# Performance work log

Measured on AMD Instinct MI355X. Metric: run time of the kernel, lower is better.

Reference implementation:

```python
import jax, jax.numpy as jnp
import numpy as np

B, N, E, C1, C2 = 8, 4096, 2048, 128, 128
DENSITY = 0.05  # incidence matrix sparsity (stored dense, as in the original)


def setup_inputs() -> dict:
    key = jax.random.key(0)
    kx, kh, kw = jax.random.split(key, 3)
    x = jax.random.normal(kx, (B, N, C1), dtype=jnp.float32)
    # binary hypergraph incidence matrix [B, n_node, n_edge]
    H = (jax.random.uniform(kh, (B, N, E)) < DENSITY).astype(jnp.float32)
    W = jax.random.normal(kw, (C1, C2), dtype=jnp.float32) * 0.02
    b = jnp.zeros((C2,), dtype=jnp.float32)
    return {"x": x, "H": H, "W": W, "b": b}


def _mean_agg(path, X):
    # path: [B, T, S], X: [B, S, D] -> mean-aggregated [B, T, D]
    out = jnp.matmul(path, X)
    s = jnp.sum(path, axis=2, keepdims=True)  # [B, T, 1]
    # 1/s with inf (s==0) masked to 0, fused as a single where
    return jnp.where(s > 0, out / s, jnp.zeros_like(out))


def reference(x, H, W, b):
    # fc: [B, N, C1] -> [B, N, C2]
    x = jnp.matmul(x, W) + b
    # v2e: aggregate node features into hyperedge features
    Ht = jnp.swapaxes(H, 1, 2)  # [B, E, N]
    e = _mean_agg(Ht, x)        # [B, E, C2]
    # e2v: aggregate hyperedge features back to nodes
    v = _mean_agg(H, e)         # [B, N, C2]
    return v
```

## Files before the change

kernel.cpp:

```cpp
#include <hip/hip_runtime.h>
#include <stdint.h>

constexpr int B_ = 8, N_ = 4096, E_ = 2048, C_ = 128;
constexpr int KT = 32;
constexpr int MT = 64;
constexpr int NJW = 2;

typedef short bf16x8 __attribute__((ext_vector_type(8)));
typedef float f32x4  __attribute__((ext_vector_type(4)));
typedef unsigned int u32x4 __attribute__((ext_vector_type(4)));

__device__ inline uint16_t bf16_rne(float f) {
    uint32_t u = __builtin_bit_cast(uint32_t, f);
    return (uint16_t)((u + 0x7FFFu + ((u >> 16) & 1u)) >> 16);
}

constexpr size_t BIT_B = (size_t)(N_ / 32) * E_;
constexpr size_t HT_E  = (size_t)B_ * BIT_B;
constexpr size_t WT_E  = (size_t)C_ * C_;
constexpr size_t EBF_E = (size_t)B_ * C_ * E_;
constexpr size_t RS_E  = (size_t)B_ * E_;
constexpr size_t RD_E  = (size_t)B_ * N_;

__global__ void pack_kernel(const float* __restrict__ H, uint32_t* __restrict__ HT,
                            uint32_t* __restrict__ HTe) {
    const int t  = threadIdx.x;
    const int eg = blockIdx.x & 7;
    const int ng = (blockIdx.x >> 3) & 127;
    const int b  = blockIdx.x >> 10;
    const int e  = eg * 256 + t;
    const float* hp = H + ((size_t)b * N_ + ng * 32) * E_ + e;
    uint32_t w = 0;
#pragma unroll
    for (int i = 0; i < 32; ++i) w |= (hp[(size_t)i * E_] > 0.5f) ? (1u << i) : 0u;
    HT[((size_t)b * (N_ / 32) + ng) * E_ + e] = w;

    const int lane  = t & 63;
    const int ebase = eg * 256 + (t >> 6) * 64;
    uint32_t val = 0;
#pragma unroll
    for (int i = 0; i < 32; ++i) {
        unsigned long long m = __ballot((w >> i) & 1u);
        uint32_t half = (lane < 32) ? (uint32_t)m : (uint32_t)(m >> 32);
        if ((lane & 31) == i) val = half;
    }
    HTe[((size_t)b * (E_ / 32) + (ebase >> 5) + (lane >> 5)) * N_ + ng * 32 + (lane & 31)] = val;
}

__global__ void prep_kernel(const float* __restrict__ W, const uint32_t* __restrict__ HT,
                            const uint32_t* __restrict__ HTe, uint16_t* __restrict__ WTb,
                            float* __restrict__ rs_e, float* __restrict__ rd_n) {
    const int blk = blockIdx.x, t = threadIdx.x;
    if (blk < 128) {
        const int i = blk * 256 + t;
        const int b = i >> 12, n = i & 4095;
        const uint32_t* p = HTe + (size_t)b * BIT_B + n;
        int s = 0;
#pragma unroll 1
        for (int ew = 0; ew < E_ / 32; ++ew) s += __popc(p[(size_t)ew * N_]);
        rd_n[i] = (s > 0) ? 0.5f / (float)s : 0.f;
    } else if (blk < 192) {
        const int i = (blk - 128) * 256 + t;
        const int b = i >> 11, e = i & 2047;
        const uint32_t* p = HT + (size_t)b * BIT_B + e;
        int s = 0;
#pragma unroll 1
        for (int ng = 0; ng < N_ / 32; ++ng) s += __popc(p[(size_t)ng * E_]);
        rs_e[i] = (s > 0) ? 0.5f / (float)s : 0.f;
    } else if (blk < 256) {
        const int i = (blk - 192) * 256 + t;
        const int c = i >> 7, k = i & 127;
        WTb[i] = bf16_rne(W[k * C_ + c]);
    }
}


#define LOADA(S, k0_) do {                                                            \
    if constexpr (MODE == 0) {                                                        \
        _Pragma("unroll")                                                             \
        for (int g = 0; g < NG; ++g) {                                                \
            const float* ap = Ax + ((size_t)batch * N_ + m0 + g * 16 + l15) * C_ + (k0_) + quad * 8; \
            const float4 f0 = *(const float4*)ap;                                     \
            const float4 f1 = *(const float4*)(ap + 4);                               \
            af##S[g*8+0]=f0.x; af##S[g*8+1]=f0.y; af##S[g*8+2]=f0.z; af##S[g*8+3]=f0.w; \
            af##S[g*8+4]=f1.x; af##S[g*8+5]=f1.y; af##S[g*8+6]=f1.z; af##S[g*8+7]=f1.w; \
        }                                                                             \
    } else {                                                                          \
        const uint32_t* p = Hp + (size_t)((k0_) >> 5) * RL + m0 + l15;                \
        _Pragma("unroll")                                                             \
        for (int g = 0; g < NG; ++g) aw##S[g] = p[g * 16];                            \
    } } while (0)

#define LOADB(S, k0_) do {                                                            \
    _Pragma("unroll")                                                                 \
    for (int j2 = 0; j2 < NJW; ++j2)                                                  \
        bq##S[j2] = *(const bf16x8*)&Bp[(size_t)((jw + j2) * 16 + l15) * K + (k0_) + quad * 8]; \
    } while (0)

#define MKFRAGS(S, A)                                                                 \
    bf16x8 A[NG];                                                                     \
    do {                                                                              \
    if constexpr (MODE == 0) {                                                        \
        _Pragma("unroll")                                                             \
        for (int g = 0; g < NG; ++g)                                                  \
            { _Pragma("unroll")                                                       \
              for (int jj = 0; jj < 8; ++jj) A[g][jj] = (short)bf16_rne(af##S[g*8+jj]); } \
    } else {                                                                          \
        const int qs = quad * 8;                                                      \
        _Pragma("unroll")                                                             \
        for (int g = 0; g < NG; ++g) {                                                \
            const uint32_t wv = aw##S[g];                                             \
            const uint32_t nb0 = (wv >> qs) & 0xFu;                                   \
            const uint32_t nb1 = (wv >> (qs + 4)) & 0xFu;                             \
            const uint32_t s0m = ((nb0 * 0x204081u) & 0x01010101u) << 6;              \
            const uint32_t s1m = ((nb1 * 0x204081u) & 0x01010101u) << 6;              \
            u32x4 qq = { __builtin_amdgcn_perm(s0m, 0u, 0x05000400u),                 \
                         __builtin_amdgcn_perm(s0m, 0u, 0x07000600u),                 \
                         __builtin_amdgcn_perm(s1m, 0u, 0x05000400u),                 \
                         __builtin_amdgcn_perm(s1m, 0u, 0x07000600u) };               \
            A[g] = __builtin_bit_cast(bf16x8, qq);                                    \
        }                                                                             \
    } } while (0)

template <int MODE>
__device__ __attribute__((always_inline))
void gemm_body(const float* __restrict__ Ax, const uint32_t* __restrict__ bits,
               const uint16_t* __restrict__ Btb, const float* __restrict__ bias,
               const float* __restrict__ rcp, uint16_t* __restrict__ outT,
               float* __restrict__ outF) {
    constexpr int K   = (MODE == 0) ? C_ : (MODE == 1) ? N_ : E_;
    constexpr int SW  = K / KT;
    constexpr int OLD = (MODE == 0) ? N_ : E_;
    constexpr int RL  = (MODE == 1) ? E_ : N_;
    constexpr int NG  = MT / 16;
    static_assert(SW >= 4 && SW % 4 == 0, "pipeline needs SW multiple of 4");

    const int t = threadIdx.x, wave = t >> 6, lane = t & 63;
    const int l15 = lane & 15, quad = lane >> 4;
    const int batch = blockIdx.x & 7;
    const int m0 = (blockIdx.x >> 3) * MT;
    const int jw = wave * NJW;

    const uint16_t* Bp = Btb + (MODE == 0 ? (size_t)0 : (size_t)batch * C_ * K);
    const uint32_t* Hp = bits + (size_t)batch * BIT_B;

    f32x4 acc[NG * NJW];
    float    af0[NG * 8], af1[NG * 8], af2[NG * 8], af3[NG * 8];
    uint32_t aw0[NG], aw1[NG], aw2[NG], aw3[NG];
    bf16x8   bq0[NJW], bq1[NJW], bq2[NJW], bq3[NJW];

    auto mfma_all = [&](const bf16x8 (&A)[NG], const bf16x8 (&bv)[NJW])
        __attribute__((always_inline)) {
#pragma unroll
        for (int j2 = 0; j2 < NJW; ++j2)
#pragma unroll
            for (int g = 0; g < NG; ++g)
                acc[g * NJW + j2] = __builtin_amdgcn_mfma_f32_16x16x32_bf16(A[g], bv[j2], acc[g * NJW + j2], 0, 0, 0);
    };

#pragma unroll
    for (int i = 0; i < NG * NJW; ++i) acc[i] = (f32x4){0.f, 0.f, 0.f, 0.f};

    LOADA(0, 0);      LOADB(0, 0);
    LOADA(1, KT);     LOADB(1, KT);
    LOADA(2, 2 * KT); LOADB(2, 2 * KT);
    LOADA(3, 3 * KT); LOADB(3, 3 * KT);

#pragma unroll 1
    for (int s = 0; s < SW - 4; s += 4) {
        { MKFRAGS(0, A0); mfma_all(A0, bq0); LOADA(0, (s + 4) * KT); LOADB(0, (s + 4) * KT); }
        { MKFRAGS(1, A1); mfma_all(A1, bq1); LOADA(1, (s + 5) * KT); LOADB(1, (s + 5) * KT); }
        { MKFRAGS(2, A2); mfma_all(A2, bq2); LOADA(2, (s + 6) * KT); LOADB(2, (s + 6) * KT); }
        { MKFRAGS(3, A3); mfma_all(A3, bq3); LOADA(3, (s + 7) * KT); LOADB(3, (s + 7) * KT); }
    }
    { MKFRAGS(0, A0); mfma_all(A0, bq0); }
    { MKFRAGS(1, A1); mfma_all(A1, bq1); }
    { MKFRAGS(2, A2); mfma_all(A2, bq2); }
    { MKFRAGS(3, A3); mfma_all(A3, bq3); }

    float mul[NG][4];
    if constexpr (MODE != 0) {
#pragma unroll
        for (int g = 0; g < NG; ++g) {
            const float4 rv = *(const float4*)&rcp[(size_t)batch * RL + m0 + g * 16 + quad * 4];
            mul[g][0] = rv.x; mul[g][1] = rv.y; mul[g][2] = rv.z; mul[g][3] = rv.w;
        }
    }
#pragma unroll
    for (int g = 0; g < NG; ++g) {
        const int row = m0 + g * 16 + quad * 4;
        if constexpr (MODE == 2) {
            float* op = outF + ((size_t)batch * N_ + row) * C_;
#pragma unroll
            for (int j2 = 0; j2 < NJW; ++j2) {
                const int c = (jw + j2) * 16 + l15;
#pragma unroll
                for (int r = 0; r < 4; ++r) op[(size_t)r * C_ + c] = acc[g * NJW + j2][r] * mul[g][r];
            }
        } else {
#pragma unroll
            for (int j2 = 0; j2 < NJW; ++j2) {
                const int c = (jw + j2) * 16 + l15;
                float v0, v1, v2, v3;
                if constexpr (MODE == 0) {
                    float bb = bias[c];
                    v0 = acc[g * NJW + j2][0] + bb; v1 = acc[g * NJW + j2][1] + bb;
                    v2 = acc[g * NJW + j2][2] + bb; v3 = acc[g * NJW + j2][3] + bb;
                } else {
                    v0 = acc[g * NJW + j2][0] * mul[g][0]; v1 = acc[g * NJW + j2][1] * mul[g][1];
                    v2 = acc[g * NJW + j2][2] * mul[g][2]; v3 = acc[g * NJW + j2][3] * mul[g][3];
                }
                uint32_t q0 = (uint32_t)bf16_rne(v0) | ((uint32_t)bf16_rne(v1) << 16);
                uint32_t q1 = (uint32_t)bf16_rne(v2) | ((uint32_t)bf16_rne(v3) << 16);
                uint16_t* op = outT + ((size_t)batch * C_ + c) * OLD + row;
                *(uint2*)op = make_uint2(q0, q1);
            }
        }
    }
}

__global__ __launch_bounds__(256, 2)
void fc_k(const float* __restrict__ Ax, const uint16_t* __restrict__ Btb,
          const float* __restrict__ bias, uint16_t* __restrict__ outT) {
    gemm_body<0>(Ax, nullptr, Btb, bias, nullptr, outT, nullptr);
}
__global__ __launch_bounds__(256, 2)
void v2e_k(const uint32_t* __restrict__ HT, const uint16_t* __restrict__ Btb,
           const float* __restrict__ rcp, uint16_t* __restrict__ outT) {
    gemm_body<1>(nullptr, HT, Btb, nullptr, rcp, outT, nullptr);
}
__global__ __launch_bounds__(256, 2)
void e2v_k(const uint32_t* __restrict__ HTe, const uint16_t* __restrict__ Btb,
           const float* __restrict__ rcp, float* __restrict__ outF) {
    gemm_body<2>(nullptr, HTe, Btb, nullptr, rcp, nullptr, outF);
}

extern "C" void kernel_launch(void* const* d_in, const int* in_sizes, int n_in,
                              void* d_out, int out_size, void* d_ws, size_t ws_size,
                              hipStream_t stream) {
    const float* x    = (const float*)d_in[0];
    const float* H    = (const float*)d_in[1];
    const float* W    = (const float*)d_in[2];
    const float* bias = (const float*)d_in[3];
    float* out = (float*)d_out;

    uint32_t* HT   = (uint32_t*)d_ws;
    uint32_t* HTe  = HT + HT_E;
    uint16_t* WTb  = (uint16_t*)(HTe + HT_E);
    uint16_t* ebfT = WTb + WT_E;
    float*    rs_e = (float*)(ebfT + EBF_E);
    float*    rd_n = rs_e + RS_E;
    uint16_t* xwbT = (uint16_t*)d_out;

    pack_kernel<<<dim3(8192), dim3(256), 0, stream>>>(H, HT, HTe);
    prep_kernel<<<dim3(256), dim3(256), 0, stream>>>(W, HT, HTe, WTb, rs_e, rd_n);
    fc_k <<<dim3(8 * (N_ / MT)), dim3(256), 0, stream>>>(x, WTb, bias, xwbT);
    v2e_k<<<dim3(8 * (E_ / MT)), dim3(256), 0, stream>>>(HT, xwbT, rs_e, ebfT);
    e2v_k<<<dim3(8 * (N_ / MT)), dim3(256), 0, stream>>>(HTe, ebfT, rd_n, out);
}
```

Baseline: 472.3 us.

## Split K across wave pairs with LDS reduction and widen per-wave N tile

Each pair of waves now splits the K dimension in half. Each wave covers four 16-column N tiles instead of two, so two column groups cover the 128 outputs. The upper-half wave writes its partial accumulators to padded shared memory, and after a barrier the lower-half wave adds them and runs the epilogue. This shortens the serial K loop per wave and lets each A fragment feed more MFMAs. In exchange it doubles the accumulator registers per wave, adds an LDS round trip plus a block barrier, and leaves half the waves idle during the epilogue.

```diff
diff --git a/kernel.cpp b/kernel.cpp
--- a/kernel.cpp
+++ b/kernel.cpp
@@ -2,9 +2,10 @@
 #include <stdint.h>
 
 constexpr int B_ = 8, N_ = 4096, E_ = 2048, C_ = 128;
-constexpr int KT = 32;
-constexpr int MT = 64;
-constexpr int NJW = 2;
+constexpr int KT  = 32;
+constexpr int MT  = 64;
+constexpr int NJW = 4;
+constexpr int LRP = 65;
 
 typedef short bf16x8 __attribute__((ext_vector_type(8)));
 typedef float f32x4  __attribute__((ext_vector_type(4)));
@@ -129,17 +130,22 @@
                const float* __restrict__ rcp, uint16_t* __restrict__ outT,
                float* __restrict__ outF) {
     constexpr int K   = (MODE == 0) ? C_ : (MODE == 1) ? N_ : E_;
-    constexpr int SW  = K / KT;
+    constexpr int KH  = K / 2;
+    constexpr int SW  = KH / KT;
     constexpr int OLD = (MODE == 0) ? N_ : E_;
     constexpr int RL  = (MODE == 1) ? E_ : N_;
     constexpr int NG  = MT / 16;
-    static_assert(SW >= 4 && SW % 4 == 0, "pipeline needs SW multiple of 4");
+    static_assert(SW == 2 || (SW >= 4 && SW % 4 == 0), "pipeline shape");
+
+    __shared__ float R[2 * 64 * LRP];
 
     const int t = threadIdx.x, wave = t >> 6, lane = t & 63;
     const int l15 = lane & 15, quad = lane >> 4;
+    const int kh = wave & 1, jg = wave >> 1;
+    const int jw = jg * NJW;
+    const int kwv = kh * KH;
     const int batch = blockIdx.x & 7;
     const int m0 = (blockIdx.x >> 3) * MT;
-    const int jw = wave * NJW;
 
     const uint16_t* Bp = Btb + (MODE == 0 ? (size_t)0 : (size_t)batch * C_ * K);
     const uint32_t* Hp = bits + (size_t)batch * BIT_B;
@@ -161,22 +167,48 @@
 #pragma unroll
     for (int i = 0; i < NG * NJW; ++i) acc[i] = (f32x4){0.f, 0.f, 0.f, 0.f};
 
-    LOADA(0, 0);      LOADB(0, 0);
-    LOADA(1, KT);     LOADB(1, KT);
-    LOADA(2, 2 * KT); LOADB(2, 2 * KT);
-    LOADA(3, 3 * KT); LOADB(3, 3 * KT);
-
+    if constexpr (SW >= 4) {
+        LOADA(0, kwv);          LOADB(0, kwv);
+        LOADA(1, kwv + KT);     LOADB(1, kwv + KT);
+        LOADA(2, kwv + 2 * KT); LOADB(2, kwv + 2 * KT);
+        LOADA(3, kwv + 3 * KT); LOADB(3, kwv + 3 * KT);
 #pragma unroll 1
-    for (int s = 0; s < SW - 4; s += 4) {
-        { MKFRAGS(0, A0); mfma_all(A0, bq0); LOADA(0, (s + 4) * KT); LOADB(0, (s + 4) * KT); }
-        { MKFRAGS(1, A1); mfma_all(A1, bq1); LOADA(1, (s + 5) * KT); LOADB(1, (s + 5) * KT); }
-        { MKFRAGS(2, A2); mfma_all(A2, bq2); LOADA(2, (s + 6) * KT); LOADB(2, (s + 6) * KT); }
-        { MKFRAGS(3, A3); mfma_all(A3, bq3); LOADA(3, (s + 7) * KT); LOADB(3, (s + 7) * KT); }
-    }
-    { MKFRAGS(0, A0); mfma_all(A0, bq0); }
-    { MKFRAGS(1, A1); mfma_all(A1, bq1); }
-    { MKFRAGS(2, A2); mfma_all(A2, bq2); }
-    { MKFRAGS(3, A3); mfma_all(A3, bq3); }
+        for (int s = 0; s < SW - 4; s += 4) {
+            { MKFRAGS(0, A0); mfma_all(A0, bq0); LOADA(0, kwv + (s + 4) * KT); LOADB(0, kwv + (s + 4) * KT); }
+            { MKFRAGS(1, A1); mfma_all(A1, bq1); LOADA(1, kwv + (s + 5) * KT); LOADB(1, kwv + (s + 5) * KT); }
+            { MKFRAGS(2, A2); mfma_all(A2, bq2); LOADA(2, kwv + (s + 6) * KT); LOADB(2, kwv + (s + 6) * KT); }
+            { MKFRAGS(3, A3); mfma_all(A3, bq3); LOADA(3, kwv + (s + 7) * KT); LOADB(3, kwv + (s + 7) * KT); }
+        }
+        { MKFRAGS(0, A0); mfma_all(A0, bq0); }
+        { MKFRAGS(1, A1); mfma_all(A1, bq1); }
+        { MKFRAGS(2, A2); mfma_all(A2, bq2); }
+        { MKFRAGS(3, A3); mfma_all(A3, bq3); }
+    } else {
+        LOADA(0, kwv);      LOADB(0, kwv);
+        LOADA(1, kwv + KT); LOADB(1, kwv + KT);
+        { MKFRAGS(0, A0); mfma_all(A0, bq0); }
+        { MKFRAGS(1, A1); mfma_all(A1, bq1); }
+    }
+
+    const int rbase = jg * 64 * LRP;
+    if (kh == 1) {
+#pragma unroll
+        for (int g = 0; g < NG; ++g)
+#pragma unroll
+            for (int j2 = 0; j2 < NJW; ++j2)
+#pragma unroll
+                for (int r = 0; r < 4; ++r)
+                    R[rbase + (g * 16 + quad * 4 + r) * LRP + j2 * 16 + l15] = acc[g * NJW + j2][r];
+    }
+    __syncthreads();
+    if (kh != 0) return;
+#pragma unroll
+    for (int g = 0; g < NG; ++g)
+#pragma unroll
+        for (int j2 = 0; j2 < NJW; ++j2)
+#pragma unroll
+            for (int r = 0; r < 4; ++r)
+                acc[g * NJW + j2][r] += R[rbase + (g * 16 + quad * 4 + r) * LRP + j2 * 16 + l15];
 
     float mul[NG][4];
     if constexpr (MODE != 0) {
```

Result: no change. 465.7 us (median of 2 runs) (-1.4%).
